# Optimization experiments

Hardware: AMD Instinct MI355X
Metric: run time of the kernel (lower is better)

Reference implementation:

```python
import jax, jax.numpy as jnp
import numpy as np

NUM_TOKENS = 4096
IN_FEATURES = 4096
OUT_FEATURES = 4096
MAX_PACKED = 4


def setup_inputs() -> dict:
    key = jax.random.key(0)
    k1, k2, k3 = jax.random.split(key, 3)
    x = jax.random.normal(k1, (NUM_TOKENS, IN_FEATURES), dtype=jnp.float32)
    weight_stacked = jax.random.normal(
        k2, (MAX_PACKED, OUT_FEATURES, IN_FEATURES), dtype=jnp.float32) * 0.02
    indices = jax.random.randint(k3, (NUM_TOKENS,), 0, MAX_PACKED, dtype=jnp.int32)
    return {"x": x, "weight_stacked": weight_stacked, "indices": indices}


def reference(x, weight_stacked, indices):
    # apply_swap: outputs[t] = x[t] @ weight_stacked[indices[t]].T
    # Grouped-GEMM expressed as E dense GEMMs with masked combine
    # (E = max_packed is a small static constant).
    E = weight_stacked.shape[0]
    out = jnp.zeros((x.shape[0], weight_stacked.shape[1]), dtype=x.dtype)
    for e in range(E):
        sel = (indices == e)[:, None].astype(x.dtype)  # [T,1]
        out = out + sel * jnp.einsum('ti,oi->to', x, weight_stacked[e])
    return out
```

## Files before the change

kernel.cpp:

```cpp
#include <hip/hip_runtime.h>

#define T 4096
#define K 4096
#define O 4096
#define E 4

#define BK 64
#define NT (K / BK)
#define MAXT 19
#define NWG (MAXT * 16)
#define MAXT128 35

typedef __attribute__((ext_vector_type(8))) short bf16x8;
typedef __attribute__((ext_vector_type(4))) float f32x4;

__device__ __forceinline__ unsigned short f2bf(float f) {
  unsigned int u = __float_as_uint(f);
  u += 0x7fffu + ((u >> 16) & 1u);
  return (unsigned short)(u >> 16);
}

__global__ void build_meta(const int* __restrict__ idx, int* __restrict__ perm,
                           int4* __restrict__ t256, int4* __restrict__ t128) {
  const int wave = threadIdx.x >> 6;
  const int lane = threadIdx.x & 63;
  __shared__ int s_off[E + 1];
  int total = 0;
  for (int t0 = 0; t0 < T; t0 += 64) {
    int e = idx[t0 + lane];
    total += __popcll(__ballot(e == wave));
  }
  if (lane == 0) s_off[wave + 1] = total;
  __syncthreads();
  if (threadIdx.x == 0) {
    s_off[0] = 0;
    for (int e = 0; e < E; e++) s_off[e + 1] += s_off[e];
  }
  __syncthreads();
  int base = s_off[wave];
  const unsigned long long below = (1ull << lane) - 1ull;
  for (int t0 = 0; t0 < T; t0 += 64) {
    int e = idx[t0 + lane];
    unsigned long long m = __ballot(e == wave);
    if (e == wave) perm[base + __popcll(m & below)] = t0 + lane;
    base += __popcll(m);
  }
  if (threadIdx.x == 0) {
    int n = 0;
    for (int e = 0; e < E; e++) {
      int s = s_off[e], c = s_off[e + 1] - s;
      for (int r = 0; r < c; r += 256)
        t256[n++] = make_int4(e, s + r, (c - r) < 256 ? (c - r) : 256, 0);
    }
    for (; n < MAXT; n++) t256[n] = make_int4(-1, 0, 0, 0);
    n = 0;
    for (int e = 0; e < E; e++) {
      int s = s_off[e], c = s_off[e + 1] - s;
      for (int r = 0; r < c; r += 128)
        t128[n++] = make_int4(e, s + r, (c - r) < 128 ? (c - r) : 128, 0);
    }
    for (; n < MAXT128; n++) t128[n] = make_int4(-1, 0, 0, 0);
  }
}

__global__ void convert_kernel(const float4* __restrict__ w4, const float* __restrict__ x,
                               const int* __restrict__ perm,
                               ushort4* __restrict__ wb4, ushort4* __restrict__ xg4) {
  const size_t NW4 = (size_t)E * O * K / 4;
  const size_t NX4 = (size_t)T * K / 4;
  const size_t stride = (size_t)gridDim.x * blockDim.x;
  for (size_t i = (size_t)blockIdx.x * blockDim.x + threadIdx.x; i < NW4 + NX4; i += stride) {
    if (i < NW4) {
      float4 v = w4[i];
      wb4[i] = make_ushort4(f2bf(v.x), f2bf(v.y), f2bf(v.z), f2bf(v.w));
    } else {
      size_t j = i - NW4;
      int p = (int)(j >> 10);
      int c = (int)(j & 1023);
      float4 v = *((const float4*)(x + (size_t)perm[p] * K) + c);
      xg4[j] = make_ushort4(f2bf(v.x), f2bf(v.y), f2bf(v.z), f2bf(v.w));
    }
  }
}

__global__ __launch_bounds__(512, 2)
void gemm8(const unsigned short* __restrict__ xg, const unsigned short* __restrict__ wbb,
           const int* __restrict__ perm, const int4* __restrict__ tiles,
           float* __restrict__ out) {
  __shared__ unsigned short lds[65536];
  const int bid = blockIdx.x;
  const int wg = (bid & 7) * (NWG / 8) + (bid >> 3);
  const int4 td = tiles[wg >> 4];
  if (td.x < 0) return;
  const int e = td.x, p0 = td.y, rc = td.z;
  const int n0 = (wg & 15) * 256;
  const int tid = threadIdx.x;
  const int wid = tid >> 6, lane = tid & 63;
  const int wr = wid >> 2, wc = wid & 3;
  const int kc4 = lane >> 4;

  const unsigned short *srcA0, *srcA1, *srcB0, *srcB1;
  {
    const unsigned short* wB = wbb + (size_t)e * O * K + (size_t)n0 * K;
    int s0 = tid, s1 = 512 + tid;
    int b0 = s0 >> 3, v0 = (s0 & 7) ^ (b0 & 7);
    int r0 = b0 * 2 + (v0 >> 2), c0 = v0 & 3;
    int b1 = s1 >> 3, v1 = (s1 & 7) ^ (b1 & 7);
    int r1 = b1 * 2 + (v1 >> 2), c1 = v1 & 3;
    int ra0 = r0 < rc ? r0 : rc - 1;
    int ra1 = r1 < rc ? r1 : rc - 1;
    srcA0 = xg + (size_t)(p0 + ra0) * K + c0 * 8;
    srcA1 = xg + (size_t)(p0 + ra1) * K + c1 * 8;
    srcB0 = wB + (size_t)r0 * K + c0 * 8;
    srcB1 = wB + (size_t)r1 * K + c1 * 8;
  }
  unsigned short* ldsw = &lds[wid * 512];

#define GLL(gp, lp) __builtin_amdgcn_global_load_lds( \
    (const __attribute__((address_space(1))) void*)(gp), \
    (__attribute__((address_space(3))) void*)(lp), 16, 0, 0)
#define STAGE_A(bo, kh, ko) do { \
    GLL(srcA0 + (ko) + (kh) * 32, ldsw + (bo) + (kh) * 8192); \
    GLL(srcA1 + (ko) + (kh) * 32, ldsw + (bo) + (kh) * 8192 + 4096); \
  } while (0)
#define STAGE_B(bo, kh, ko) do { \
    GLL(srcB0 + (ko) + (kh) * 32, ldsw + (bo) + 16384 + (kh) * 8192); \
    GLL(srcB1 + (ko) + (kh) * 32, ldsw + (bo) + 16384 + (kh) * 8192 + 4096); \
  } while (0)

  int aoff[2][4], boff[4];
#pragma unroll
  for (int mh = 0; mh < 2; ++mh)
#pragma unroll
    for (int mi = 0; mi < 4; ++mi) {
      int r = wr * 128 + mh * 64 + mi * 16 + (lane & 15);
      aoff[mh][mi] = (((r >> 1) << 3) + (((((r & 1) << 2) | kc4)) ^ ((r >> 1) & 7))) * 8;
    }
#pragma unroll
  for (int ni = 0; ni < 4; ++ni) {
    int r = wc * 64 + ni * 16 + (lane & 15);
    boff[ni] = (((r >> 1) << 3) + (((((r & 1) << 2) | kc4)) ^ ((r >> 1) & 7))) * 8;
  }

  f32x4 acc[8][4] = {};
  bf16x8 af[4], bf[4];

#define LOAD_AF(bo, ks, mh) do { _Pragma("unroll") \
    for (int mi = 0; mi < 4; ++mi) \
      af[mi] = *(const bf16x8*)&lds[(bo) + (ks) * 8192 + aoff[mh][mi]]; } while (0)
#define LOAD_BF(bo, ks) do { _Pragma("unroll") \
    for (int ni = 0; ni < 4; ++ni) \
      bf[ni] = *(const bf16x8*)&lds[(bo) + 16384 + (ks) * 8192 + boff[ni]]; } while (0)
#define MFMA16(mh) do { _Pragma("unroll") \
    for (int mi = 0; mi < 4; ++mi) _Pragma("unroll") \
      for (int ni = 0; ni < 4; ++ni) \
        acc[(mh) * 4 + mi][ni] = __builtin_amdgcn_mfma_f32_16x16x32_bf16( \
            af[mi], bf[ni], acc[(mh) * 4 + mi][ni], 0, 0, 0); } while (0)
#define BAR() do { __builtin_amdgcn_s_barrier(); asm volatile("" ::: "memory"); } while (0)
#define LGKM0() asm volatile("s_waitcnt lgkmcnt(0)" ::: "memory")
#define VM4() asm volatile("s_waitcnt vmcnt(4)" ::: "memory")

  STAGE_A(0, 0, 0); STAGE_B(0, 0, 0);
  STAGE_A(0, 1, 0); STAGE_B(0, 1, 0);
  VM4(); BAR();

  for (int t = 0; t < NT; ++t) {
    const int cur = (t & 1) << 15;
    const int nxt = cur ^ 32768;
    const int ko = (t + 1 < NT ? t + 1 : t) * BK;
    LOAD_AF(cur, 0, 0); LOAD_BF(cur, 0);
    STAGE_A(nxt, 0, ko);
    BAR(); LGKM0();
    __builtin_amdgcn_s_setprio(1); MFMA16(0); __builtin_amdgcn_s_setprio(0);
    BAR();
    LOAD_AF(cur, 0, 1);
    STAGE_B(nxt, 0, ko);
    BAR(); LGKM0();
    __builtin_amdgcn_s_setprio(1); MFMA16(1); __builtin_amdgcn_s_setprio(0);
    VM4(); BAR();
    LOAD_AF(cur, 1, 0); LOAD_BF(cur, 1);
    STAGE_A(nxt, 1, ko);
    BAR(); LGKM0();
    __builtin_amdgcn_s_setprio(1); MFMA16(0); __builtin_amdgcn_s_setprio(0);
    BAR();
    LOAD_AF(cur, 1, 1);
    STAGE_B(nxt, 1, ko);
    BAR(); LGKM0();
    __builtin_amdgcn_s_setprio(1); MFMA16(1); __builtin_amdgcn_s_setprio(0);
    VM4(); BAR();
  }

#pragma unroll
  for (int mh = 0; mh < 2; ++mh)
#pragma unroll
    for (int mi = 0; mi < 4; ++mi) {
      const int rbase = wr * 128 + mh * 64 + mi * 16 + (lane >> 4) * 4;
#pragma unroll
      for (int reg = 0; reg < 4; ++reg) {
        const int pr = rbase + reg;
        if (pr < rc) {
          float* orow = out + (size_t)perm[p0 + pr] * O + n0 + wc * 64 + (lane & 15);
#pragma unroll
          for (int ni = 0; ni < 4; ++ni) orow[ni * 16] = acc[mh * 4 + mi][ni][reg];
        }
      }
    }
}

__global__ __launch_bounds__(256)
void gemm_fb(const float* __restrict__ xf, const float* __restrict__ wf,
             const int* __restrict__ perm, const int4* __restrict__ tiles,
             float* __restrict__ out) {
  __shared__ unsigned short lds_a[128 * 64];
  __shared__ unsigned short lds_b[128 * 64];
  const int4 td = tiles[blockIdx.x];
  if (td.x < 0) return;
  const int e = td.x, p0 = td.y, rc = td.z;
  const int n0 = blockIdx.y * 128;
  const int wave = threadIdx.x >> 6, lane = threadIdx.x & 63;
  const int wr = wave >> 1, wc = wave & 1;
  f32x4 acc[4][4] = {};
  const float* wf_base = wf + (size_t)e * O * K + (size_t)n0 * K;
  for (int k0 = 0; k0 < K; k0 += 64) {
    if (k0) __syncthreads();
#pragma unroll
    for (int i = 0; i < 8; i++) {
      int l4 = i * 256 + (int)threadIdx.x;
      int row = l4 >> 4;
      int c4 = (l4 & 15) << 2;
      int ra = row < rc ? row : (rc - 1);
      const float4 va = *(const float4*)(xf + (size_t)perm[p0 + ra] * K + k0 + c4);
      *(ushort4*)&lds_a[row * 64 + c4] = make_ushort4(f2bf(va.x), f2bf(va.y), f2bf(va.z), f2bf(va.w));
      const float4 vb = *(const float4*)(wf_base + (size_t)row * K + k0 + c4);
      *(ushort4*)&lds_b[row * 64 + c4] = make_ushort4(f2bf(vb.x), f2bf(vb.y), f2bf(vb.z), f2bf(vb.w));
    }
    __syncthreads();
#pragma unroll
    for (int ks = 0; ks < 2; ks++) {
      bf16x8 a2[4], b2[4];
#pragma unroll
      for (int mi = 0; mi < 4; mi++)
        a2[mi] = *(const bf16x8*)&lds_a[(wr * 64 + mi * 16 + (lane & 15)) * 64 + ks * 32 + (lane >> 4) * 8];
#pragma unroll
      for (int ni = 0; ni < 4; ni++)
        b2[ni] = *(const bf16x8*)&lds_b[(wc * 64 + ni * 16 + (lane & 15)) * 64 + ks * 32 + (lane >> 4) * 8];
#pragma unroll
      for (int mi = 0; mi < 4; mi++)
#pragma unroll
        for (int ni = 0; ni < 4; ni++)
          acc[mi][ni] = __builtin_amdgcn_mfma_f32_16x16x32_bf16(a2[mi], b2[ni], acc[mi][ni], 0, 0, 0);
    }
  }
#pragma unroll
  for (int mi = 0; mi < 4; mi++) {
    const int rb = wr * 64 + mi * 16 + (lane >> 4) * 4;
#pragma unroll
    for (int reg = 0; reg < 4; reg++) {
      const int rt = rb + reg;
      if (rt < rc) {
        float* orow = out + (size_t)perm[p0 + rt] * O + n0 + wc * 64 + (lane & 15);
#pragma unroll
        for (int ni = 0; ni < 4; ni++) orow[ni * 16] = acc[mi][ni][reg];
      }
    }
  }
}

extern "C" void kernel_launch(void* const* d_in, const int* in_sizes, int n_in,
                              void* d_out, int out_size, void* d_ws, size_t ws_size,
                              hipStream_t stream) {
  const float* x = (const float*)d_in[0];
  const float* w = (const float*)d_in[1];
  const int* idx = (const int*)d_in[2];
  float* out = (float*)d_out;
  char* ws = (char*)d_ws;

  int* perm = (int*)ws;
  int4* t256 = (int4*)(ws + 16384);
  int4* t128 = (int4*)(ws + 18432);
  unsigned short* xg = (unsigned short*)(ws + 32768);
  unsigned short* wb = (unsigned short*)(ws + 32768 + (size_t)T * K * 2);
  const size_t need = 32768 + (size_t)T * K * 2 + (size_t)E * O * K * 2;

  build_meta<<<1, 256, 0, stream>>>(idx, perm, t256, t128);
  if (ws_size >= need) {
    convert_kernel<<<2048, 256, 0, stream>>>((const float4*)w, x, perm,
                                             (ushort4*)wb, (ushort4*)xg);
    gemm8<<<NWG, 512, 0, stream>>>(xg, wb, perm, t256, out);
  } else {
    gemm_fb<<<dim3(MAXT128, 32), 256, 0, stream>>>(x, w, perm, t128, out);
  }
}
```

Baseline: 324.9 us.

## Use persistent 256-block stream-K schedule with split-K atomics for remainder tiles

Replaces the one-block-per-tile grouped GEMM with 256 persistent blocks. Each block first takes one full 256x256 output tile, then handles K-segments of the leftover tiles, which are split across blocks and combined with atomic adds into an output zeroed beforehand. The aim is to balance the wave-quantization tail when the tile count is not a multiple of the CU count. The cost is an extra zeroing kernel, float atomics on partial tiles, and a more complex schedule built in the metadata kernel.

```diff
diff --git a/kernel.cpp b/kernel.cpp
--- a/kernel.cpp
+++ b/kernel.cpp
@@ -4,11 +4,7 @@
 #define K 4096
 #define O 4096
 #define E 4
-
 #define BK 64
-#define NT (K / BK)
-#define MAXT 19
-#define NWG (MAXT * 16)
 #define MAXT128 35
 
 typedef __attribute__((ext_vector_type(8))) short bf16x8;
@@ -21,15 +17,16 @@
 }
 
 __global__ void build_meta(const int* __restrict__ idx, int* __restrict__ perm,
-                           int4* __restrict__ t256, int4* __restrict__ t128) {
+                           int* __restrict__ meta, int4* __restrict__ t256,
+                           int4* __restrict__ t128, int4* __restrict__ sched) {
   const int wave = threadIdx.x >> 6;
   const int lane = threadIdx.x & 63;
   __shared__ int s_off[E + 1];
+  __shared__ int rtE[20], rtP[20], rtC[20];
+  __shared__ int r_sh;
   int total = 0;
-  for (int t0 = 0; t0 < T; t0 += 64) {
-    int e = idx[t0 + lane];
-    total += __popcll(__ballot(e == wave));
-  }
+  for (int t0 = 0; t0 < T; t0 += 64)
+    total += __popcll(__ballot(idx[t0 + lane] == wave));
   if (lane == 0) s_off[wave + 1] = total;
   __syncthreads();
   if (threadIdx.x == 0) {
@@ -49,18 +46,51 @@
     int n = 0;
     for (int e = 0; e < E; e++) {
       int s = s_off[e], c = s_off[e + 1] - s;
-      for (int r = 0; r < c; r += 256)
-        t256[n++] = make_int4(e, s + r, (c - r) < 256 ? (c - r) : 256, 0);
-    }
-    for (; n < MAXT; n++) t256[n] = make_int4(-1, 0, 0, 0);
-    n = 0;
+      for (int ro = 0; ro < c; ro += 256) {
+        rtE[n] = e; rtP[n] = s + ro; rtC[n] = (c - ro) < 256 ? (c - ro) : 256; n++;
+      }
+    }
+    r_sh = n;
+    meta[0] = n * 16;
+    int n1 = 0;
     for (int e = 0; e < E; e++) {
       int s = s_off[e], c = s_off[e + 1] - s;
-      for (int r = 0; r < c; r += 128)
-        t128[n++] = make_int4(e, s + r, (c - r) < 128 ? (c - r) : 128, 0);
-    }
-    for (; n < MAXT128; n++) t128[n] = make_int4(-1, 0, 0, 0);
-  }
+      for (int ro = 0; ro < c; ro += 128)
+        t128[n1++] = make_int4(e, s + ro, (c - ro) < 128 ? (c - ro) : 128, 0);
+    }
+    for (; n1 < MAXT128; n1++) t128[n1] = make_int4(-1, 0, 0, 0);
+  }
+  __syncthreads();
+  const int r = r_sh;
+  for (int i = threadIdx.x; i < 16 * r; i += 256)
+    t256[i] = make_int4(rtE[i >> 4], rtP[i >> 4], rtC[i >> 4], (i & 15) * 256);
+  {
+    const int b = threadIdx.x;
+    const int ru = r - 16;
+    sched[b * 3 + 0] = make_int4((b & 7) * 32 + (b >> 3), 0, 16, 0);
+    int sgi = 1, u0 = b * ru, u1 = u0 + ru;
+    while (u0 < u1) {
+      int tI = 256 + (u0 >> 4), q0 = u0 & 15;
+      int avail = 16 - q0, want = u1 - u0;
+      int take = want < avail ? want : avail;
+      sched[b * 3 + sgi] = make_int4(tI, q0, take, 0);
+      sgi++; u0 += take;
+    }
+    for (; sgi < 3; sgi++) sched[b * 3 + sgi] = make_int4(-1, 0, 0, 0);
+  }
+}
+
+__global__ void zero_rem(const int* __restrict__ meta, const int4* __restrict__ t256,
+                         const int* __restrict__ perm, float* __restrict__ out) {
+  const int ntiles = meta[0];
+  const int tI = 256 + (int)blockIdx.x / 16;
+  if (tI >= ntiles) return;
+  const int4 td = t256[tI];
+  const int rt = (blockIdx.x & 15) * 16 + ((int)threadIdx.x >> 4);
+  if (rt >= td.z) return;
+  float4* p = (float4*)(out + (size_t)perm[td.y + rt] * O + td.w) + (threadIdx.x & 15) * 4;
+  const float4 z = {0.f, 0.f, 0.f, 0.f};
+  p[0] = z; p[1] = z; p[2] = z; p[3] = z;
 }
 
 __global__ void convert_kernel(const float4* __restrict__ w4, const float* __restrict__ x,
@@ -84,36 +114,15 @@
 }
 
 __global__ __launch_bounds__(512, 2)
-void gemm8(const unsigned short* __restrict__ xg, const unsigned short* __restrict__ wbb,
-           const int* __restrict__ perm, const int4* __restrict__ tiles,
-           float* __restrict__ out) {
+void gemm8p(const unsigned short* __restrict__ xg, const unsigned short* __restrict__ wbb,
+            const int* __restrict__ perm, const int4* __restrict__ t256,
+            const int4* __restrict__ sched, float* __restrict__ out) {
   __shared__ unsigned short lds[65536];
   const int bid = blockIdx.x;
-  const int wg = (bid & 7) * (NWG / 8) + (bid >> 3);
-  const int4 td = tiles[wg >> 4];
-  if (td.x < 0) return;
-  const int e = td.x, p0 = td.y, rc = td.z;
-  const int n0 = (wg & 15) * 256;
   const int tid = threadIdx.x;
   const int wid = tid >> 6, lane = tid & 63;
   const int wr = wid >> 2, wc = wid & 3;
   const int kc4 = lane >> 4;
-
-  const unsigned short *srcA0, *srcA1, *srcB0, *srcB1;
-  {
-    const unsigned short* wB = wbb + (size_t)e * O * K + (size_t)n0 * K;
-    int s0 = tid, s1 = 512 + tid;
-    int b0 = s0 >> 3, v0 = (s0 & 7) ^ (b0 & 7);
-    int r0 = b0 * 2 + (v0 >> 2), c0 = v0 & 3;
-    int b1 = s1 >> 3, v1 = (s1 & 7) ^ (b1 & 7);
-    int r1 = b1 * 2 + (v1 >> 2), c1 = v1 & 3;
-    int ra0 = r0 < rc ? r0 : rc - 1;
-    int ra1 = r1 < rc ? r1 : rc - 1;
-    srcA0 = xg + (size_t)(p0 + ra0) * K + c0 * 8;
-    srcA1 = xg + (size_t)(p0 + ra1) * K + c1 * 8;
-    srcB0 = wB + (size_t)r0 * K + c0 * 8;
-    srcB1 = wB + (size_t)r1 * K + c1 * 8;
-  }
   unsigned short* ldsw = &lds[wid * 512];
 
 #define GLL(gp, lp) __builtin_amdgcn_global_load_lds( \
@@ -127,24 +136,6 @@
     GLL(srcB0 + (ko) + (kh) * 32, ldsw + (bo) + 16384 + (kh) * 8192); \
     GLL(srcB1 + (ko) + (kh) * 32, ldsw + (bo) + 16384 + (kh) * 8192 + 4096); \
   } while (0)
-
-  int aoff[2][4], boff[4];
-#pragma unroll
-  for (int mh = 0; mh < 2; ++mh)
-#pragma unroll
-    for (int mi = 0; mi < 4; ++mi) {
-      int r = wr * 128 + mh * 64 + mi * 16 + (lane & 15);
-      aoff[mh][mi] = (((r >> 1) << 3) + (((((r & 1) << 2) | kc4)) ^ ((r >> 1) & 7))) * 8;
-    }
-#pragma unroll
-  for (int ni = 0; ni < 4; ++ni) {
-    int r = wc * 64 + ni * 16 + (lane & 15);
-    boff[ni] = (((r >> 1) << 3) + (((((r & 1) << 2) | kc4)) ^ ((r >> 1) & 7))) * 8;
-  }
-
-  f32x4 acc[8][4] = {};
-  bf16x8 af[4], bf[4];
-
 #define LOAD_AF(bo, ks, mh) do { _Pragma("unroll") \
     for (int mi = 0; mi < 4; ++mi) \
       af[mi] = *(const bf16x8*)&lds[(bo) + (ks) * 8192 + aoff[mh][mi]]; } while (0)
@@ -159,52 +150,116 @@
 #define BAR() do { __builtin_amdgcn_s_barrier(); asm volatile("" ::: "memory"); } while (0)
 #define LGKM0() asm volatile("s_waitcnt lgkmcnt(0)" ::: "memory")
 #define VM4() asm volatile("s_waitcnt vmcnt(4)" ::: "memory")
-
-  STAGE_A(0, 0, 0); STAGE_B(0, 0, 0);
-  STAGE_A(0, 1, 0); STAGE_B(0, 1, 0);
-  VM4(); BAR();
-
-  for (int t = 0; t < NT; ++t) {
-    const int cur = (t & 1) << 15;
-    const int nxt = cur ^ 32768;
-    const int ko = (t + 1 < NT ? t + 1 : t) * BK;
-    LOAD_AF(cur, 0, 0); LOAD_BF(cur, 0);
-    STAGE_A(nxt, 0, ko);
-    BAR(); LGKM0();
-    __builtin_amdgcn_s_setprio(1); MFMA16(0); __builtin_amdgcn_s_setprio(0);
-    BAR();
-    LOAD_AF(cur, 0, 1);
-    STAGE_B(nxt, 0, ko);
-    BAR(); LGKM0();
-    __builtin_amdgcn_s_setprio(1); MFMA16(1); __builtin_amdgcn_s_setprio(0);
+#define VM0() asm volatile("s_waitcnt vmcnt(0)" ::: "memory")
+
+  int aoff[2][4], boff[4];
+#pragma unroll
+  for (int mh = 0; mh < 2; ++mh)
+#pragma unroll
+    for (int mi = 0; mi < 4; ++mi) {
+      int r = wr * 128 + mh * 64 + mi * 16 + (lane & 15);
+      aoff[mh][mi] = (((r >> 1) << 3) + (((((r & 1) << 2) | kc4)) ^ ((r >> 1) & 7))) * 8;
+    }
+#pragma unroll
+  for (int ni = 0; ni < 4; ++ni) {
+    int r = wc * 64 + ni * 16 + (lane & 15);
+    boff[ni] = (((r >> 1) << 3) + (((((r & 1) << 2) | kc4)) ^ ((r >> 1) & 7))) * 8;
+  }
+
+  for (int sg = 0; sg < 3; ++sg) {
+    const int4 sd = sched[bid * 3 + sg];
+    if (sd.x < 0) break;
+    const int4 td = t256[sd.x];
+    const int e = td.x, p0 = td.y, rc = td.z, n0 = td.w;
+    const int kt0 = sd.y << 2;
+    const int nt = sd.z << 2;
+
+    const unsigned short *srcA0, *srcA1, *srcB0, *srcB1;
+    {
+      const unsigned short* wB = wbb + (size_t)e * O * K + (size_t)n0 * K;
+      int s0 = tid, s1 = 512 + tid;
+      int b0 = s0 >> 3, v0 = (s0 & 7) ^ (b0 & 7);
+      int r0 = b0 * 2 + (v0 >> 2), c0 = v0 & 3;
+      int b1 = s1 >> 3, v1 = (s1 & 7) ^ (b1 & 7);
+      int r1 = b1 * 2 + (v1 >> 2), c1 = v1 & 3;
+      int ra0 = r0 < rc ? r0 : rc - 1;
+      int ra1 = r1 < rc ? r1 : rc - 1;
+      srcA0 = xg + (size_t)(p0 + ra0) * K + c0 * 8;
+      srcA1 = xg + (size_t)(p0 + ra1) * K + c1 * 8;
+      srcB0 = wB + (size_t)r0 * K + c0 * 8;
+      srcB1 = wB + (size_t)r1 * K + c1 * 8;
+    }
+
+    f32x4 acc[8][4] = {};
+    bf16x8 af[4], bf[4];
+
+    const int kb = kt0 << 6;
+    STAGE_A(0, 0, kb); STAGE_B(0, 0, kb);
+    STAGE_A(0, 1, kb); STAGE_B(0, 1, kb);
     VM4(); BAR();
-    LOAD_AF(cur, 1, 0); LOAD_BF(cur, 1);
-    STAGE_A(nxt, 1, ko);
-    BAR(); LGKM0();
-    __builtin_amdgcn_s_setprio(1); MFMA16(0); __builtin_amdgcn_s_setprio(0);
-    BAR();
-    LOAD_AF(cur, 1, 1);
-    STAGE_B(nxt, 1, ko);
-    BAR(); LGKM0();
-    __builtin_amdgcn_s_setprio(1); MFMA16(1); __builtin_amdgcn_s_setprio(0);
-    VM4(); BAR();
-  }
-
-#pragma unroll
-  for (int mh = 0; mh < 2; ++mh)
-#pragma unroll
-    for (int mi = 0; mi < 4; ++mi) {
-      const int rbase = wr * 128 + mh * 64 + mi * 16 + (lane >> 4) * 4;
-#pragma unroll
-      for (int reg = 0; reg < 4; ++reg) {
-        const int pr = rbase + reg;
-        if (pr < rc) {
-          float* orow = out + (size_t)perm[p0 + pr] * O + n0 + wc * 64 + (lane & 15);
-#pragma unroll
-          for (int ni = 0; ni < 4; ++ni) orow[ni * 16] = acc[mh * 4 + mi][ni][reg];
+
+    for (int t = 0; t < nt; ++t) {
+      const int cur = (t & 1) << 15;
+      const int nxt = cur ^ 32768;
+      const int ko = ((t + 1 < nt ? t + 1 : t) + kt0) << 6;
+      LOAD_AF(cur, 0, 0); LOAD_BF(cur, 0);
+      STAGE_A(nxt, 0, ko);
+      BAR(); LGKM0();
+      __builtin_amdgcn_s_setprio(1); MFMA16(0); __builtin_amdgcn_s_setprio(0);
+      BAR();
+      LOAD_AF(cur, 0, 1);
+      STAGE_B(nxt, 0, ko);
+      BAR(); LGKM0();
+      __builtin_amdgcn_s_setprio(1); MFMA16(1); __builtin_amdgcn_s_setprio(0);
+      VM4(); BAR();
+      LOAD_AF(cur, 1, 0); LOAD_BF(cur, 1);
+      STAGE_A(nxt, 1, ko);
+      BAR(); LGKM0();
+      __builtin_amdgcn_s_setprio(1); MFMA16(0); __builtin_amdgcn_s_setprio(0);
+      BAR();
+      LOAD_AF(cur, 1, 1);
+      STAGE_B(nxt, 1, ko);
+      BAR(); LGKM0();
+      __builtin_amdgcn_s_setprio(1); MFMA16(1); __builtin_amdgcn_s_setprio(0);
+      VM4(); BAR();
+    }
+    VM0();
+
+    if (sd.z == 16) {
+#pragma unroll
+      for (int mh = 0; mh < 2; ++mh)
+#pragma unroll
+        for (int mi = 0; mi < 4; ++mi) {
+          const int rbase = wr * 128 + mh * 64 + mi * 16 + (lane >> 4) * 4;
+#pragma unroll
+          for (int reg = 0; reg < 4; ++reg) {
+            const int pr = rbase + reg;
+            if (pr < rc) {
+              float* orow = out + (size_t)perm[p0 + pr] * O + n0 + wc * 64 + (lane & 15);
+#pragma unroll
+              for (int ni = 0; ni < 4; ++ni) orow[ni * 16] = acc[mh * 4 + mi][ni][reg];
+            }
+          }
         }
-      }
-    }
+    } else {
+#pragma unroll
+      for (int mh = 0; mh < 2; ++mh)
+#pragma unroll
+        for (int mi = 0; mi < 4; ++mi) {
+          const int rbase = wr * 128 + mh * 64 + mi * 16 + (lane >> 4) * 4;
+#pragma unroll
+          for (int reg = 0; reg < 4; ++reg) {
+            const int pr = rbase + reg;
+            if (pr < rc) {
+              float* orow = out + (size_t)perm[p0 + pr] * O + n0 + wc * 64 + (lane & 15);
+#pragma unroll
+              for (int ni = 0; ni < 4; ++ni)
+                unsafeAtomicAdd(&orow[ni * 16], acc[mh * 4 + mi][ni][reg]);
+            }
+          }
+        }
+    }
+  }
 }
 
 __global__ __launch_bounds__(256)
@@ -276,17 +331,20 @@
   char* ws = (char*)d_ws;
 
   int* perm = (int*)ws;
-  int4* t256 = (int4*)(ws + 16384);
-  int4* t128 = (int4*)(ws + 18432);
-  unsigned short* xg = (unsigned short*)(ws + 32768);
-  unsigned short* wb = (unsigned short*)(ws + 32768 + (size_t)T * K * 2);
-  const size_t need = 32768 + (size_t)T * K * 2 + (size_t)E * O * K * 2;
-
-  build_meta<<<1, 256, 0, stream>>>(idx, perm, t256, t128);
+  int* meta = (int*)(ws + 16384);
+  int4* t256 = (int4*)(ws + 16640);
+  int4* t128 = (int4*)(ws + 22528);
+  int4* sched = (int4*)(ws + 24576);
+  unsigned short* xg = (unsigned short*)(ws + 65536);
+  unsigned short* wb = xg + (size_t)T * K;
+  const size_t need = 65536 + (size_t)T * K * 2 + (size_t)E * O * K * 2;
+
+  build_meta<<<1, 256, 0, stream>>>(idx, perm, meta, t256, t128, sched);
   if (ws_size >= need) {
+    zero_rem<<<768, 256, 0, stream>>>(meta, t256, perm, out);
     convert_kernel<<<2048, 256, 0, stream>>>((const float4*)w, x, perm,
                                              (ushort4*)wb, (ushort4*)xg);
-    gemm8<<<NWG, 512, 0, stream>>>(xg, wb, perm, t256, out);
+    gemm8p<<<256, 512, 0, stream>>>(xg, wb, perm, t256, sched, out);
   } else {
     gemm_fb<<<dim3(MAXT128, 32), 256, 0, stream>>>(x, w, perm, t128, out);
   }
```

Result: faster. 278.6 us (-14.2%).
